# Kernel tuning notes

Measured on AMD Instinct MI355X. Metric: run time of the kernel, lower is better.

## Reference

```python
import jax, jax.numpy as jnp
import numpy as np

NUM_TIMES = 1024  # times are drawn from [0, 1024), used as fixed segment count
N = 16777216


def setup_inputs() -> dict:
    key = jax.random.key(0)
    k1, k2, k3 = jax.random.split(key, 3)
    outs = jax.random.normal(k1, (N,), dtype=jnp.float32)
    T_E = jax.random.randint(k2, (N,), 0, 2, dtype=jnp.int32)
    T_T = jax.random.randint(k3, (N,), 0, NUM_TIMES, dtype=jnp.int32)
    return {"outs": outs, "T_E": T_E, "T_T": T_T}


def reference(outs, T_E, T_T):
    # E[E > 0] = 1  -> binary event indicator
    E = (T_E > 0).astype(outs.dtype)
    # Y_label_T = |T_T| ; integer times act directly as segment ids
    seg_ids = jnp.abs(T_T)
    Obs = jnp.sum(E)
    # log of running sum of hazards: log(cumsum(exp(yhat)))
    y_hat_cumsum = jnp.log(jnp.cumsum(jnp.exp(outs)))
    # original segment_max initializes accumulator at 0, so it is clipped below at 0;
    # jnp.maximum also neutralizes -inf fill for empty segments (count=0 there anyway)
    seg_max = jnp.maximum(
        jax.ops.segment_max(y_hat_cumsum, seg_ids, num_segments=NUM_TIMES), 0.0
    )
    seg_cnt = jax.ops.segment_sum(E, seg_ids, num_segments=NUM_TIMES)
    loss_s2 = jnp.sum(seg_max * seg_cnt)
    loss_s1 = jnp.sum(outs * E)
    return (loss_s2 - loss_s1) / Obs
```

## Files before the change

### kernel.cpp

```cpp
#include <hip/hip_runtime.h>

#define NUM_SEGS 1024
#define CHUNK_LOG 13
#define CHUNK (1 << CHUNK_LOG)
#define SUBCH 4
#define SUPER (CHUNK * SUBCH)
#define BLK 512
#define NWAVE (BLK / 64)
#define NBATCH 16
#define PDEPTH 6
#define SEGBLK 256

__device__ __forceinline__ float waveReduceSumF(float v) {
#pragma unroll
    for (int off = 32; off > 0; off >>= 1) v += __shfl_down(v, off, 64);
    return v;
}
__device__ __forceinline__ double waveReduceSumD(double v) {
#pragma unroll
    for (int off = 32; off > 0; off >>= 1) v += __shfl_down(v, off, 64);
    return v;
}
__device__ __forceinline__ unsigned waveReduceSumU(unsigned v) {
#pragma unroll
    for (int off = 32; off > 0; off >>= 1) v += __shfl_down(v, off, 64);
    return v;
}
__device__ __forceinline__ int waveReduceMaxI(int v) {
#pragma unroll
    for (int off = 32; off > 0; off >>= 1) {
        const int o = __shfl_down(v, off, 64);
        v = o > v ? o : v;
    }
    return v;
}

__global__ void init_kernel(unsigned* __restrict__ seg_cnt,
                            float* __restrict__ csums, int nChunks,
                            unsigned* __restrict__ obs,
                            double* __restrict__ loss1,
                            double* __restrict__ loss2,
                            unsigned* __restrict__ done) {
    const int t = blockIdx.x * blockDim.x + threadIdx.x;
    if (t < NUM_SEGS) seg_cnt[t] = 0u;
    if (t < nChunks) csums[t] = 0.f;
    if (t == 0) { obs[0] = 0u; loss1[0] = 0.0; loss2[0] = 0.0; done[0] = 0u; }
}

__global__ __launch_bounds__(BLK, 2) void pass1_kernel(
    const float* __restrict__ outs, const int* __restrict__ te,
    const int* __restrict__ tt, int N, int nChunks,
    float* __restrict__ csums, unsigned* __restrict__ seg_cnt,
    unsigned* __restrict__ obs, double* __restrict__ loss1) {
    __shared__ unsigned hist[NUM_SEGS];
    __shared__ float redF[NWAVE];
    __shared__ unsigned redU[NWAVE];

    for (int t = threadIdx.x; t < NUM_SEGS; t += BLK) hist[t] = 0u;
    __syncthreads();

    const int lane = threadIdx.x & 63;
    const int wid = threadIdx.x >> 6;
    const int superBase = blockIdx.x * SUPER;

    float sE[SUBCH] = {0.f, 0.f, 0.f, 0.f};
    float sumOE = 0.f;
    unsigned cntE = 0u;

    if (superBase + SUPER <= N) {
        const int i0 = superBase + ((int)threadIdx.x << 2);
        float4 O[PDEPTH];
        int4 E[PDEPTH], S[PDEPTH];

#define LOADB(b, sl)                                                        \
    do {                                                                    \
        const int _i = i0 + (b) * (BLK * 4);                                \
        O[sl] = *reinterpret_cast<const float4*>(outs + _i);                \
        E[sl] = *reinterpret_cast<const int4*>(te + _i);                    \
        S[sl] = *reinterpret_cast<const int4*>(tt + _i);                    \
    } while (0)

#pragma unroll
        for (int b = 0; b < PDEPTH; ++b) LOADB(b, b);

#pragma unroll
        for (int b = 0; b < NBATCH; ++b) {
            if (b + PDEPTH < NBATCH) LOADB(b + PDEPTH, (b + PDEPTH) % PDEPTH);
            __builtin_amdgcn_sched_barrier(0);
            {
                const int sl = b % PDEPTH;
                const float4 o = O[sl];
                const int4 ev = E[sl];
                const int4 sv = S[sl];
                sE[b >> 2] += (__expf(o.x) + __expf(o.y)) +
                              (__expf(o.z) + __expf(o.w));
                const int s0 = sv.x < 0 ? -sv.x : sv.x;
                const int s1 = sv.y < 0 ? -sv.y : sv.y;
                const int s2 = sv.z < 0 ? -sv.z : sv.z;
                const int s3 = sv.w < 0 ? -sv.w : sv.w;
                if (ev.x > 0) { cntE++; sumOE += o.x; atomicAdd(&hist[s0], 1u); }
                if (ev.y > 0) { cntE++; sumOE += o.y; atomicAdd(&hist[s1], 1u); }
                if (ev.z > 0) { cntE++; sumOE += o.z; atomicAdd(&hist[s2], 1u); }
                if (ev.w > 0) { cntE++; sumOE += o.w; atomicAdd(&hist[s3], 1u); }
            }
        }
#undef LOADB

        const int c0 = superBase >> CHUNK_LOG;
#pragma unroll
        for (int k = 0; k < SUBCH; ++k) {
            const float w = waveReduceSumF(sE[k]);
            if (lane == 0) atomicAdd(&csums[c0 + k], w);
        }
    } else {
        for (int k = 0; k < SUBCH; ++k) {
            const int cbase = superBase + k * CHUNK;
            if (cbase >= N) break;
            const int end = (cbase + CHUNK < N) ? cbase + CHUNK : N;
            float s = 0.f;
            for (int i = cbase + (int)threadIdx.x; i < end; i += BLK) {
                const float o = outs[i];
                const int e = te[i];
                int sg = tt[i]; sg = sg < 0 ? -sg : sg;
                s += __expf(o);
                if (e > 0) { cntE++; sumOE += o; atomicAdd(&hist[sg], 1u); }
            }
            const float w = waveReduceSumF(s);
            if (lane == 0 && w != 0.f) atomicAdd(&csums[cbase >> CHUNK_LOG], w);
        }
    }

    __syncthreads();

    for (int t = threadIdx.x; t < NUM_SEGS; t += BLK) {
        const unsigned h = hist[t];
        if (h) atomicAdd(&seg_cnt[t], h);
    }

    const float wOE = waveReduceSumF(sumOE);
    const unsigned wC = waveReduceSumU(cntE);
    if (lane == 0) { redF[wid] = wOE; redU[wid] = wC; }
    __syncthreads();
    if (threadIdx.x == 0) {
        float oe = 0.f; unsigned c = 0u;
#pragma unroll
        for (int j = 0; j < NWAVE; ++j) { oe += redF[j]; c += redU[j]; }
        atomicAdd(loss1, (double)oe);
        atomicAdd(obs, c);
    }
}

__global__ __launch_bounds__(SEGBLK) void seg_final_kernel(
    const float* __restrict__ outs, const int* __restrict__ tt,
    const float* __restrict__ csums, const unsigned* __restrict__ seg_cnt,
    const double* __restrict__ loss1, double* __restrict__ loss2,
    const unsigned* __restrict__ obs, unsigned* __restrict__ done,
    float* __restrict__ out, int N, int nChunks) {
    __shared__ double redD[SEGBLK / 64];
    __shared__ float redF[SEGBLK / 64];
    __shared__ int redI[SEGBLK / 64];
    __shared__ int s_li;

    const int t = blockIdx.x;
    const unsigned cnt = seg_cnt[t];
    const int lane = threadIdx.x & 63, wid = threadIdx.x >> 6;

    if (cnt != 0u) {
        int c = nChunks - 1;
        int LI = -1;
        for (;;) {
            const int base = c << CHUNK_LOG;
            const int end = (base + CHUNK < N) ? base + CHUNK : N;
            const int span = end - base;
            const int qspan = span & ~3;
            int li = -1;
            for (int i = base + ((int)threadIdx.x << 2); i < base + qspan;
                 i += SEGBLK * 4) {
                const int4 sv = *reinterpret_cast<const int4*>(tt + i);
                const int s0 = sv.x < 0 ? -sv.x : sv.x;
                const int s1 = sv.y < 0 ? -sv.y : sv.y;
                const int s2 = sv.z < 0 ? -sv.z : sv.z;
                const int s3 = sv.w < 0 ? -sv.w : sv.w;
                if (s3 == t) li = i + 3;
                else if (s2 == t) li = i + 2;
                else if (s1 == t) li = i + 1;
                else if (s0 == t) li = i;
            }
            for (int i = base + qspan + (int)threadIdx.x; i < end; i += SEGBLK) {
                int s = tt[i]; s = s < 0 ? -s : s;
                if (s == t && i > li) li = i;
            }
            li = waveReduceMaxI(li);
            if (lane == 0) redI[wid] = li;
            __syncthreads();
            if (threadIdx.x == 0) {
                int m = redI[0];
#pragma unroll
                for (int j = 1; j < SEGBLK / 64; ++j) m = redI[j] > m ? redI[j] : m;
                s_li = m;
            }
            __syncthreads();
            LI = s_li;
            if (LI >= 0 || --c < 0) break;
        }

        if (LI >= 0) {
            double p = 0.0;
            for (int j = threadIdx.x; j < c; j += SEGBLK) p += (double)csums[j];
            p = waveReduceSumD(p);
            if (lane == 0) redD[wid] = p;

            const int base = c << CHUNK_LOG;
            float fs = 0.f;
            for (int i = base + (int)threadIdx.x; i <= LI; i += SEGBLK)
                fs += __expf(outs[i]);
            fs = waveReduceSumF(fs);
            if (lane == 0) redF[wid] = fs;
            __syncthreads();
            if (threadIdx.x == 0) {
                double pre = 0.0;
                float fsum = 0.f;
#pragma unroll
                for (int j = 0; j < SEGBLK / 64; ++j) { pre += redD[j]; fsum += redF[j]; }
                double sm = log(pre + (double)fsum);
                if (sm < 0.0) sm = 0.0;
                atomicAdd(loss2, sm * (double)cnt);
            }
        }
    }

    if (threadIdx.x == 0) {
        __threadfence();
        const unsigned d = atomicAdd(done, 1u);
        if (d == (unsigned)(gridDim.x - 1)) {
            const double l2 = atomicAdd(loss2, 0.0);
            const double l1 = *(volatile const double*)loss1;
            const unsigned o = *(volatile const unsigned*)obs;
            out[0] = (float)((l2 - l1) / (double)o);
        }
    }
}

extern "C" void kernel_launch(void* const* d_in, const int* in_sizes, int n_in,
                              void* d_out, int out_size, void* d_ws, size_t ws_size,
                              hipStream_t stream) {
    const float* outs = (const float*)d_in[0];
    const int* te = (const int*)d_in[1];
    const int* tt = (const int*)d_in[2];
    const int N = in_sizes[0];
    float* out = (float*)d_out;

    const int nChunks = (N + CHUNK - 1) / CHUNK;

    char* ws = (char*)d_ws;
    double* d_loss1 = (double*)ws;
    double* d_loss2 = d_loss1 + 1;
    float* d_csums = (float*)(ws + 16);
    unsigned* d_segcnt = (unsigned*)(d_csums + nChunks);
    unsigned* d_obs = d_segcnt + NUM_SEGS;
    unsigned* d_done = d_obs + 1;

    const int initThreads = (nChunks > NUM_SEGS ? nChunks : NUM_SEGS);
    init_kernel<<<(initThreads + 255) / 256, 256, 0, stream>>>(
        d_segcnt, d_csums, nChunks, d_obs, d_loss1, d_loss2, d_done);
    const int nSuper = (N + SUPER - 1) / SUPER;
    pass1_kernel<<<nSuper, BLK, 0, stream>>>(outs, te, tt, N, nChunks, d_csums,
                                             d_segcnt, d_obs, d_loss1);
    seg_final_kernel<<<NUM_SEGS, SEGBLK, 0, stream>>>(
        outs, tt, d_csums, d_segcnt, d_loss1, d_loss2, d_obs, d_done, out, N,
        nChunks);
}
```

Before: 227.8 us.

## Pipeline pass1 loads with inline-asm global loads and explicit vmcnt waits

Replaces compiler-scheduled vectorized loads with inline-asm global_load_dwordx4 issued PDEPTH batches ahead, using explicit s_waitcnt vmcnt counters so each batch waits only for its own loads. Block size drops from 512 to 256 and subchunks per block from 4 to 2, which keeps per-block work at NBATCH batches while launching more, smaller blocks. The goal is to keep more memory requests in flight and stop the compiler from inserting conservative full waits. Hand-written waitcnt values must exactly match the issue order, and any mismatch or extra compiler-emitted vector memory op could produce incorrect reads.

```diff
diff --git a/kernel.cpp b/kernel.cpp
--- a/kernel.cpp
+++ b/kernel.cpp
@@ -3,9 +3,9 @@
 #define NUM_SEGS 1024
 #define CHUNK_LOG 13
 #define CHUNK (1 << CHUNK_LOG)
-#define SUBCH 4
+#define SUBCH 2
 #define SUPER (CHUNK * SUBCH)
-#define BLK 512
+#define BLK 256
 #define NWAVE (BLK / 64)
 #define NBATCH 16
 #define PDEPTH 6
@@ -63,7 +63,7 @@
     const int wid = threadIdx.x >> 6;
     const int superBase = blockIdx.x * SUPER;
 
-    float sE[SUBCH] = {0.f, 0.f, 0.f, 0.f};
+    float sE[SUBCH] = {0.f, 0.f};
     float sumOE = 0.f;
     unsigned cntE = 0u;
 
@@ -72,39 +72,54 @@
         float4 O[PDEPTH];
         int4 E[PDEPTH], S[PDEPTH];
 
-#define LOADB(b, sl)                                                        \
-    do {                                                                    \
-        const int _i = i0 + (b) * (BLK * 4);                                \
-        O[sl] = *reinterpret_cast<const float4*>(outs + _i);                \
-        E[sl] = *reinterpret_cast<const int4*>(te + _i);                    \
-        S[sl] = *reinterpret_cast<const int4*>(tt + _i);                    \
+#define ISSUE(b)                                                              \
+    do {                                                                      \
+        const float* _po = outs + (i0 + (b) * (BLK * 4));                     \
+        const int* _pe = te + (i0 + (b) * (BLK * 4));                         \
+        const int* _pt = tt + (i0 + (b) * (BLK * 4));                         \
+        asm volatile("global_load_dwordx4 %0, %1, off"                        \
+                     : "=&v"(O[(b) % PDEPTH]) : "v"(_po));                    \
+        asm volatile("global_load_dwordx4 %0, %1, off"                        \
+                     : "=&v"(E[(b) % PDEPTH]) : "v"(_pe));                    \
+        asm volatile("global_load_dwordx4 %0, %1, off"                        \
+                     : "=&v"(S[(b) % PDEPTH]) : "v"(_pt));                    \
     } while (0)
 
-#pragma unroll
-        for (int b = 0; b < PDEPTH; ++b) LOADB(b, b);
-
-#pragma unroll
-        for (int b = 0; b < NBATCH; ++b) {
-            if (b + PDEPTH < NBATCH) LOADB(b + PDEPTH, (b + PDEPTH) % PDEPTH);
-            __builtin_amdgcn_sched_barrier(0);
-            {
-                const int sl = b % PDEPTH;
-                const float4 o = O[sl];
-                const int4 ev = E[sl];
-                const int4 sv = S[sl];
-                sE[b >> 2] += (__expf(o.x) + __expf(o.y)) +
-                              (__expf(o.z) + __expf(o.w));
-                const int s0 = sv.x < 0 ? -sv.x : sv.x;
-                const int s1 = sv.y < 0 ? -sv.y : sv.y;
-                const int s2 = sv.z < 0 ? -sv.z : sv.z;
-                const int s3 = sv.w < 0 ? -sv.w : sv.w;
-                if (ev.x > 0) { cntE++; sumOE += o.x; atomicAdd(&hist[s0], 1u); }
-                if (ev.y > 0) { cntE++; sumOE += o.y; atomicAdd(&hist[s1], 1u); }
-                if (ev.z > 0) { cntE++; sumOE += o.z; atomicAdd(&hist[s2], 1u); }
-                if (ev.w > 0) { cntE++; sumOE += o.w; atomicAdd(&hist[s3], 1u); }
-            }
-        }
-#undef LOADB
+#define CONSUME(b)                                                            \
+    do {                                                                      \
+        const float4 o = O[(b) % PDEPTH];                                     \
+        const int4 ev = E[(b) % PDEPTH];                                      \
+        const int4 sv = S[(b) % PDEPTH];                                      \
+        sE[(b) >> 3] += (__expf(o.x) + __expf(o.y)) +                         \
+                        (__expf(o.z) + __expf(o.w));                          \
+        const int s0 = sv.x < 0 ? -sv.x : sv.x;                               \
+        const int s1 = sv.y < 0 ? -sv.y : sv.y;                               \
+        const int s2 = sv.z < 0 ? -sv.z : sv.z;                               \
+        const int s3 = sv.w < 0 ? -sv.w : sv.w;                               \
+        if (ev.x > 0) { cntE++; sumOE += o.x; atomicAdd(&hist[s0], 1u); }     \
+        if (ev.y > 0) { cntE++; sumOE += o.y; atomicAdd(&hist[s1], 1u); }     \
+        if (ev.z > 0) { cntE++; sumOE += o.z; atomicAdd(&hist[s2], 1u); }     \
+        if (ev.w > 0) { cntE++; sumOE += o.w; atomicAdd(&hist[s3], 1u); }     \
+    } while (0)
+
+#define STEP(b, wc)                                                           \
+    do {                                                                      \
+        asm volatile("s_waitcnt vmcnt(" #wc ")");                             \
+        __builtin_amdgcn_sched_barrier(0);                                    \
+        CONSUME(b);                                                           \
+        __builtin_amdgcn_sched_barrier(0);                                    \
+        if ((b) + PDEPTH < NBATCH) ISSUE((b) + PDEPTH);                       \
+    } while (0)
+
+        ISSUE(0); ISSUE(1); ISSUE(2); ISSUE(3); ISSUE(4); ISSUE(5);
+        STEP(0, 15);  STEP(1, 15);  STEP(2, 15);  STEP(3, 15);
+        STEP(4, 15);  STEP(5, 15);  STEP(6, 15);  STEP(7, 15);
+        STEP(8, 15);  STEP(9, 15);  STEP(10, 15);
+        STEP(11, 12); STEP(12, 9);  STEP(13, 6);  STEP(14, 3);  STEP(15, 0);
+
+#undef STEP
+#undef CONSUME
+#undef ISSUE
 
         const int c0 = superBase >> CHUNK_LOG;
 #pragma unroll
```

Result: slower. 239.1 us (+4.9%).
